# Kernel tuning notes

Hardware: AMD Instinct MI355X
Metric: run time of the kernel (lower is better)

Reference implementation:

```python
import jax, jax.numpy as jnp
import numpy as np

V = 50257   # vocab_size
D = 128     # embed_dim
B = 1024    # batch of center words
C = 10      # context window size


def setup_inputs() -> dict:
    key = jax.random.key(0)
    ks = jax.random.split(key, 12)
    s = 0.05  # small init scale for linear weights
    return {
        "center_id": jax.random.randint(ks[0], (B,), 0, V),
        "context_ids": jax.random.randint(ks[1], (B, C), 0, V),
        "epsilon": jax.random.normal(ks[2], (D,), dtype=jnp.float32),
        # embedding tables init uniform(-1, 1) as in the torch module
        "emb": jax.random.uniform(ks[3], (V, D), minval=-1.0, maxval=1.0, dtype=jnp.float32),
        "prior_means": jax.random.uniform(ks[4], (V, D), minval=-1.0, maxval=1.0, dtype=jnp.float32),
        "prior_vars": jax.random.uniform(ks[5], (V, D), minval=-1.0, maxval=1.0, dtype=jnp.float32),
        "W_enc": jax.random.normal(ks[6], (2 * D, 2 * D), dtype=jnp.float32) * s,
        "b_enc": jnp.zeros((2 * D,), dtype=jnp.float32),
        "W_mean": jax.random.normal(ks[7], (2 * D, D), dtype=jnp.float32) * s,
        "b_mean": jnp.zeros((D,), dtype=jnp.float32),
        "W_var": jax.random.normal(ks[8], (2 * D, D), dtype=jnp.float32) * s,
        "b_var": jnp.zeros((D,), dtype=jnp.float32),
        "W_vocab": jax.random.normal(ks[9], (D, V), dtype=jnp.float32) * s,
        "b_vocab": jnp.zeros((V,), dtype=jnp.float32),
    }


def reference(center_id, context_ids, epsilon, emb, prior_means, prior_vars,
              W_enc, b_enc, W_mean, b_mean, W_var, b_var, W_vocab, b_vocab):
    ce = emb[center_id]                       # [B, D]
    cx = emb[context_ids]                     # [B, C, D]
    enc_in = jnp.concatenate(
        [jnp.broadcast_to(ce[:, None, :], cx.shape), cx], axis=-1)  # [B, C, 2D]
    h = jax.nn.relu(enc_in @ W_enc + b_enc).sum(axis=1)  # [B, 2D]
    mean = h @ W_mean + b_mean                           # [B, D]
    var = jax.nn.softplus(h @ W_var + b_var)             # [B, D] (diag cov s0)
    z = mean + jnp.exp(var / 2.0) * epsilon              # single shared epsilon [D]
    logits = z @ W_vocab + b_vocab                        # [B, V]
    logp = jax.nn.log_softmax(logits, axis=1)             # log(categorical)

    pm = prior_means[center_id]                           # m1 [B, D]
    pv = jax.nn.softplus(prior_vars[center_id])           # diag cov s1 [B, D]
    diff = pm - mean
    # closed-form diagonal Gaussian KL, identical math to the
    # trace/inverse/det formulation over diagflat matrices in the source
    kl = 0.5 * jnp.sum(var / pv + diff * diff / pv - 1.0
                       + jnp.log(pv) - jnp.log(var), axis=1)  # [B]

    # reconstruction: sum_k log categorical[i, context_ids[i, k]]
    rec = jnp.take_along_axis(logp, context_ids, axis=1).sum(axis=1)  # [B]

    return jnp.mean(rec - kl)
```

## Files before the change

kernel.cpp:

```cpp
#include <hip/hip_runtime.h>
#include <math.h>

#define VV 50257
#define VPAD 50304
#define DD 128
#define BB 1024
#define CC 10

typedef short bf16x8 __attribute__((ext_vector_type(8)));
typedef float f32x4 __attribute__((ext_vector_type(4)));

__device__ inline float bf2f(unsigned short u) {
    return __uint_as_float(((unsigned)u) << 16);
}
__device__ inline unsigned short f2bf(float f) {
    unsigned u = __float_as_uint(f);
    unsigned r = ((u >> 16) & 1) + 0x7FFF;
    return (unsigned short)((u + r) >> 16);
}


__global__ __launch_bounds__(256) void k_prep0(
    const float* __restrict__ W_enc, const float* __restrict__ W_mean,
    const float* __restrict__ W_var, unsigned short* __restrict__ WeP,
    unsigned short* __restrict__ Wmv)
{
    __shared__ float tl[256][17];
    const int bid = blockIdx.x, tid = threadIdx.x;

    if (bid < 16) {
        const int jg = bid;
#pragma unroll
        for (int i = 0; i < 16; ++i) {
            int idx = i * 256 + tid;
            int k = idx >> 4, j = idx & 15;
            tl[k][j] = W_enc[(size_t)k * 256 + jg * 16 + j];
        }
        __syncthreads();
#pragma unroll
        for (int i = 0; i < 2; ++i) {
            int c = i * 256 + tid;
            int l15 = c & 15, q = (c >> 4) & 3, kI = c >> 6;
            bf16x8 o;
#pragma unroll
            for (int e = 0; e < 8; ++e)
                o[e] = (short)f2bf(tl[kI * 32 + q * 8 + e][l15]);
            *(bf16x8*)(WeP + (((size_t)jg * 8 + kI) * 64 + q * 16 + l15) * 8) = o;
        }
        return;
    }

    const int b4 = bid - 16;
#pragma unroll
    for (int i = 0; i < 32; ++i) {
        int idx = b4 * 8192 + i * 256 + tid;
        unsigned short m = f2bf(W_mean[idx]);
        unsigned short v = f2bf(W_var[idx]);
        *(ushort2*)(Wmv + (size_t)idx * 2) = make_ushort2(m, v);
    }
}

#define AS_STRIDE 520
__global__ __launch_bounds__(256) void k_main(
    const int* __restrict__ center_id, const int* __restrict__ context_ids,
    const float* __restrict__ emb, const unsigned short* __restrict__ WeP,
    const float* __restrict__ b_enc, const float* __restrict__ Wv,
    unsigned short* __restrict__ WvP, unsigned short* __restrict__ enc_relu)
{
    __shared__ __align__(16) unsigned char smraw[50688];
    const int bid = blockIdx.x, tid = threadIdx.x;

    if (bid >= 320) {
        float (*tile)[65] = (float (*)[65])smraw;
        const int s = bid - 320;
        const int v0 = s * 64;
#pragma unroll
        for (int i = 0; i < 32; ++i) {
            int idx = tid + i * 256;
            int k = idx >> 6, j = idx & 63;
            int v = v0 + j;
            tile[k][j] = (v < VV) ? Wv[(size_t)k * VV + v] : 0.f;
        }
        __syncthreads();
#pragma unroll
        for (int i = 0; i < 4; ++i) {
            int c = i * 256 + tid;
            int l15 = c & 15, q = (c >> 4) & 3, kI = (c >> 6) & 3, g = c >> 8;
            bf16x8 o;
#pragma unroll
            for (int e = 0; e < 8; ++e)
                o[e] = (short)f2bf(tile[kI * 32 + q * 8 + e][g * 16 + l15]);
            size_t vg = (size_t)s * 4 + g;
            *(bf16x8*)(WvP + ((vg * 4 + kI) * 64 + q * 16 + l15) * 8) = o;
        }
        return;
    }

    unsigned short* As = (unsigned short*)smraw;
    unsigned short (*Cs)[136] = (unsigned short (*)[136])(smraw + 33280);

    const int lane = tid & 63;
    const int wid  = tid >> 6;
    const int wm   = wid & 1;
    const int wn   = wid >> 1;
    const int quad = lane >> 4;
    const int l15  = lane & 15;

    const int bt = bid & 15;
    const int c  = (bid >> 4) % 10;
    const int zt = bid / 160;
    const int b0 = bt * 64;
    const int n0 = zt * 128;

    const int rlane = tid >> 4;
    const int c8    = tid & 15;
    const int kIc   = c8 >> 2, qc = c8 & 3;
#pragma unroll
    for (int p = 0; p < 4; ++p) {
        int r = p * 16 + rlane;
        int rid_ce = center_id[b0 + r];
        int rid_cx = context_ids[(b0 + r) * CC + c];
        const float* s0 = emb + (size_t)rid_ce * 128 + c8 * 8;
        const float* s1 = emb + (size_t)rid_cx * 128 + c8 * 8;
        float4 a0 = *(const float4*)s0, a1 = *(const float4*)(s0 + 4);
        float4 b0v = *(const float4*)s1, b1v = *(const float4*)(s1 + 4);
        bf16x8 oa, ob;
        oa[0] = (short)f2bf(a0.x); oa[1] = (short)f2bf(a0.y);
        oa[2] = (short)f2bf(a0.z); oa[3] = (short)f2bf(a0.w);
        oa[4] = (short)f2bf(a1.x); oa[5] = (short)f2bf(a1.y);
        oa[6] = (short)f2bf(a1.z); oa[7] = (short)f2bf(a1.w);
        ob[0] = (short)f2bf(b0v.x); ob[1] = (short)f2bf(b0v.y);
        ob[2] = (short)f2bf(b0v.z); ob[3] = (short)f2bf(b0v.w);
        ob[4] = (short)f2bf(b1v.x); ob[5] = (short)f2bf(b1v.y);
        ob[6] = (short)f2bf(b1v.z); ob[7] = (short)f2bf(b1v.w);
        *(bf16x8*)(As + (size_t)(p * 8 + kIc) * AS_STRIDE + (qc * 16 + rlane) * 8) = oa;
        *(bf16x8*)(As + (size_t)(p * 8 + kIc + 4) * AS_STRIDE + (qc * 16 + rlane) * 8) = ob;
    }
    __syncthreads();

    float benc[4];
#pragma unroll
    for (int nt = 0; nt < 4; ++nt)
        benc[nt] = b_enc[n0 + wn * 64 + nt * 16 + l15];

    f32x4 acc[2][4];
#pragma unroll
    for (int mt = 0; mt < 2; ++mt)
#pragma unroll
        for (int nt = 0; nt < 4; ++nt) acc[mt][nt] = (f32x4){0.f, 0.f, 0.f, 0.f};

#pragma unroll
    for (int kI = 0; kI < 8; ++kI) {
        bf16x8 a[2], b[4];
#pragma unroll
        for (int mt = 0; mt < 2; ++mt)
            a[mt] = *(const bf16x8*)(As + (size_t)((wm * 2 + mt) * 8 + kI) * AS_STRIDE + lane * 8);
#pragma unroll
        for (int nt = 0; nt < 4; ++nt) {
            size_t jg = (size_t)zt * 8 + wn * 4 + nt;
            b[nt] = *(const bf16x8*)(WeP + ((jg * 8 + kI) * 64 + lane) * 8);
        }
#pragma unroll
        for (int mt = 0; mt < 2; ++mt)
#pragma unroll
            for (int nt = 0; nt < 4; ++nt)
                acc[mt][nt] = __builtin_amdgcn_mfma_f32_16x16x32_bf16(
                    a[mt], b[nt], acc[mt][nt], 0, 0, 0);
    }

#pragma unroll
    for (int mt = 0; mt < 2; ++mt)
#pragma unroll
        for (int nt = 0; nt < 4; ++nt) {
            int col = wn * 64 + nt * 16 + l15;
#pragma unroll
            for (int reg = 0; reg < 4; ++reg) {
                int row = wm * 32 + mt * 16 + quad * 4 + reg;
                Cs[row][col] = f2bf(fmaxf(acc[mt][nt][reg] + benc[nt], 0.f));
            }
        }
    __syncthreads();
#pragma unroll
    for (int i = 0; i < 4; ++i) {
        int ch = i * 256 + tid;
        int row = ch >> 4, cc = ch & 15;
        bf16x8 v = *(const bf16x8*)&Cs[row][cc * 8];
        *(bf16x8*)(enc_relu + ((size_t)(b0 + row) * CC + c) * 256 + n0 + cc * 8) = v;
    }
}

__global__ __launch_bounds__(256) void k_latent(
    const unsigned short* __restrict__ enc_relu, const unsigned short* __restrict__ Wmv,
    const float* __restrict__ b_mean, const float* __restrict__ b_var,
    const float* __restrict__ epsilon,
    const int* __restrict__ center_id, const int* __restrict__ context_ids,
    const unsigned short* __restrict__ WvP, const float* __restrict__ bv,
    const float* __restrict__ prior_means, const float* __restrict__ prior_vars,
    unsigned short* __restrict__ z_pack, float* __restrict__ kl,
    float* __restrict__ ctxsum, float* __restrict__ out)
{
    __shared__ __align__(16) float hs[256];
    __shared__ float mpart[128], vpart[128];
    __shared__ float red[2];
    __shared__ float credp[CC][2];
    const int tid = threadIdx.x;
    const int b = blockIdx.x;

    if (b == 0 && tid == 0) out[0] = 0.f;

    {
        float s0 = 0.f;
#pragma unroll
        for (int c = 0; c < CC; ++c)
            s0 += bf2f(enc_relu[((size_t)b * CC + c) * 256 + tid]);
        hs[tid] = s0;
    }
    __syncthreads();

    const int d = tid & 127;
    const int half = tid >> 7;
    float m  = half ? 0.f : b_mean[d];
    float vr = half ? 0.f : b_var[d];
    const int kbase = half << 7;
    for (int k0 = 0; k0 < 128; k0 += 4) {
        float4 h4 = *(const float4*)&hs[kbase + k0];
#pragma unroll
        for (int kk = 0; kk < 4; ++kk) {
            float hk = ((const float*)&h4)[kk];
            ushort2 u = *(const ushort2*)(Wmv + ((size_t)(kbase + k0 + kk) * 128 + d) * 2);
            m  += hk * bf2f(u.x);
            vr += hk * bf2f(u.y);
        }
    }
    if (half) { mpart[d] = m; vpart[d] = vr; }
    __syncthreads();

    if (!half) {
        const int wid = tid >> 6;
        m  += mpart[d];
        vr += vpart[d];

        float var = (vr > 20.f) ? vr : log1pf(__expf(vr));
        float zd = m + __expf(0.5f * var) * epsilon[d];
        unsigned short zu = f2bf(zd);
        const int kIz = d >> 5, qz = (d >> 3) & 3, ez = d & 7;
        {
            const int bg = b >> 4, l15b = b & 15;
            z_pack[(((size_t)(bg * 4 + kIz)) * 64 + qz * 16 + l15b) * 8 + ez] = zu;
        }
        float zb = bf2f(zu);

        int cid = center_id[b];
        float pm  = prior_means[(size_t)cid * 128 + d];
        float pvr = prior_vars[(size_t)cid * 128 + d];
        float pv  = (pvr > 20.f) ? pvr : log1pf(__expf(pvr));
        float diff = pm - m;
        float t = var / pv + diff * diff / pv - 1.f + logf(pv) - logf(var);
#pragma unroll
        for (int off = 32; off; off >>= 1) t += __shfl_down(t, off, 64);
        if ((tid & 63) == 0) red[wid] = t;

        int cids[CC];
#pragma unroll
        for (int p = 0; p < CC; ++p) cids[p] = context_ids[b * CC + p];
        float cs[CC];
#pragma unroll
        for (int p = 0; p < CC; ++p) {
            int vg = cids[p] >> 4, l15v = cids[p] & 15;
            float w = bf2f(WvP[(((size_t)(vg * 4 + kIz)) * 64 + qz * 16 + l15v) * 8 + ez]);
            cs[p] = zb * w;
        }
#pragma unroll
        for (int p = 0; p < CC; ++p) {
#pragma unroll
            for (int off = 32; off; off >>= 1) cs[p] += __shfl_down(cs[p], off, 64);
        }
        if ((tid & 63) == 0) {
#pragma unroll
            for (int p = 0; p < CC; ++p) credp[p][wid] = cs[p];
        }
    }
    __syncthreads();
    if (tid == 0) {
        kl[b] = 0.5f * (red[0] + red[1]);
        float c = 0.f;
        int cid0;
#pragma unroll
        for (int p = 0; p < CC; ++p) {
            cid0 = context_ids[b * CC + p];
            c += credp[p][0] + credp[p][1] + bv[cid0];
        }
        ctxsum[b] = c;
    }
}

__global__ __launch_bounds__(256) void k_lse(
    const unsigned short* __restrict__ z_pack, const unsigned short* __restrict__ WvP,
    const float* __restrict__ bv, float* __restrict__ partial)
{
    __shared__ float pl[2][128][20];
    const int x = blockIdx.x + 8 * blockIdx.y;
    if (x >= 393) return;
    const int mg = blockIdx.z;

    const int tid  = threadIdx.x;
    const int lane = tid & 63;
    const int wid  = tid >> 6;
    const int wm   = wid & 1;
    const int wn   = wid >> 1;
    const int quad = lane >> 4;
    const int l15  = lane & 15;
    const int n0   = x * 128;

    bf16x8 bfr[4][4];
#pragma unroll
    for (int nt = 0; nt < 4; ++nt) {
        size_t vg = (size_t)x * 8 + wn * 4 + nt;
#pragma unroll
        for (int kI = 0; kI < 4; ++kI)
            bfr[nt][kI] = *(const bf16x8*)(WvP + ((vg * 4 + kI) * 64 + lane) * 8);
    }

    float bvf[4];
#pragma unroll
    for (int nt = 0; nt < 4; ++nt) {
        int n = n0 + wn * 64 + nt * 16 + l15;
        bvf[nt] = (n < VV) ? bv[n] : -__builtin_huge_valf();
    }

#pragma unroll
    for (int mi = 0; mi < 2; ++mi) {
        const int mi_g = mg * 2 + mi;

        f32x4 acc[4][4];
#pragma unroll
        for (int mt = 0; mt < 4; ++mt)
#pragma unroll
            for (int nt = 0; nt < 4; ++nt) acc[mt][nt] = (f32x4){0.f, 0.f, 0.f, 0.f};

#pragma unroll
        for (int kI = 0; kI < 4; ++kI) {
            bf16x8 afr[4];
#pragma unroll
            for (int mt = 0; mt < 4; ++mt) {
                size_t bg = (size_t)mi_g * 8 + wm * 4 + mt;
                afr[mt] = *(const bf16x8*)(z_pack + ((bg * 4 + kI) * 64 + lane) * 8);
            }
#pragma unroll
            for (int mt = 0; mt < 4; ++mt)
#pragma unroll
                for (int nt = 0; nt < 4; ++nt)
                    acc[mt][nt] = __builtin_amdgcn_mfma_f32_16x16x32_bf16(
                        afr[mt], bfr[nt][kI], acc[mt][nt], 0, 0, 0);
        }

#pragma unroll
        for (int mt = 0; mt < 4; ++mt)
#pragma unroll
            for (int reg = 0; reg < 4; ++reg) {
                float s = 0.f;
#pragma unroll
                for (int nt = 0; nt < 4; ++nt)
                    s += __expf(acc[mt][nt][reg] + bvf[nt]);
                pl[wn][wm * 64 + mt * 16 + quad * 4 + reg][l15] = s;
            }
        __syncthreads();
        if (tid < 128) {
            const float* p0 = &pl[0][tid][0];
            const float* p1 = &pl[1][tid][0];
            float4 a0 = *(const float4*)(p0);
            float4 a1 = *(const float4*)(p0 + 4);
            float4 a2 = *(const float4*)(p0 + 8);
            float4 a3 = *(const float4*)(p0 + 12);
            float4 b0 = *(const float4*)(p1);
            float4 b1 = *(const float4*)(p1 + 4);
            float4 b2 = *(const float4*)(p1 + 8);
            float4 b3 = *(const float4*)(p1 + 12);
            float tot = (a0.x + a0.y + a0.z + a0.w) + (a1.x + a1.y + a1.z + a1.w)
                      + (a2.x + a2.y + a2.z + a2.w) + (a3.x + a3.y + a3.z + a3.w)
                      + (b0.x + b0.y + b0.z + b0.w) + (b1.x + b1.y + b1.z + b1.w)
                      + (b2.x + b2.y + b2.z + b2.w) + (b3.x + b3.y + b3.z + b3.w);
            partial[(size_t)x * 1024 + mi_g * 128 + tid] = tot;
        }
        __syncthreads();
    }
}

__global__ __launch_bounds__(256) void k_reduce(
    const float* __restrict__ partial, const float* __restrict__ ctxsum,
    const float* __restrict__ kl, float* __restrict__ out)
{
    __shared__ float bred[4];
    const int tid = threadIdx.x;
    const int row = blockIdx.x * 16 + (tid >> 4);
    const int part = tid & 15;

    float s = 0.f;
    for (int vb = part; vb < 393; vb += 16)
        s += partial[(size_t)vb * 1024 + row];
    s += __shfl_xor(s, 1, 64);
    s += __shfl_xor(s, 2, 64);
    s += __shfl_xor(s, 4, 64);
    s += __shfl_xor(s, 8, 64);

    float v = 0.f;
    if (part == 0)
        v = ctxsum[row] - 10.f * logf(s) - kl[row];
    v += __shfl_xor(v, 16, 64);
    v += __shfl_xor(v, 32, 64);
    if ((tid & 63) == 0) bred[tid >> 6] = v;
    __syncthreads();
    if (tid == 0)
        atomicAdd(out, (bred[0] + bred[1] + bred[2] + bred[3]) * (1.f / 1024.f));
}

extern "C" void kernel_launch(void* const* d_in, const int* in_sizes, int n_in,
                              void* d_out, int out_size, void* d_ws, size_t ws_size,
                              hipStream_t stream)
{
    const int*   center_id   = (const int*)d_in[0];
    const int*   context_ids = (const int*)d_in[1];
    const float* epsilon     = (const float*)d_in[2];
    const float* emb         = (const float*)d_in[3];
    const float* prior_means = (const float*)d_in[4];
    const float* prior_vars  = (const float*)d_in[5];
    const float* W_enc       = (const float*)d_in[6];
    const float* b_enc       = (const float*)d_in[7];
    const float* W_mean      = (const float*)d_in[8];
    const float* b_mean      = (const float*)d_in[9];
    const float* W_var       = (const float*)d_in[10];
    const float* b_var       = (const float*)d_in[11];
    const float* W_vocab     = (const float*)d_in[12];
    const float* b_vocab     = (const float*)d_in[13];

    float* out = (float*)d_out;
    char*  ws  = (char*)d_ws;

    size_t off = 0;
    unsigned short* WvP      = (unsigned short*)(ws + off); off += 12877824;
    unsigned short* WeP      = (unsigned short*)(ws + off); off += 131072;
    unsigned short* Wmv      = (unsigned short*)(ws + off); off += 131072;
    unsigned short* z_pack   = (unsigned short*)(ws + off); off += 262144;
    unsigned short* enc_relu = (unsigned short*)(ws + off); off += 5242880;
    float*          kl       = (float*)(ws + off);          off += 4096;
    float*          ctxsum   = (float*)(ws + off);          off += 4096;
    float*          partial  = (float*)(ws + off);          off += 1609728;

    k_prep0<<<20, 256, 0, stream>>>(W_enc, W_mean, W_var, WeP, Wmv);
    k_main<<<1106, 256, 0, stream>>>(center_id, context_ids, emb, WeP, b_enc,
                                     W_vocab, WvP, enc_relu);
    k_latent<<<1024, 256, 0, stream>>>(enc_relu, Wmv, b_mean, b_var, epsilon,
                                       center_id, context_ids, WvP, b_vocab,
                                       prior_means, prior_vars, z_pack, kl,
                                       ctxsum, out);
    k_lse<<<dim3(8, 50, 4), 256, 0, stream>>>(z_pack, WvP, b_vocab, partial);
    k_reduce<<<64, 256, 0, stream>>>(partial, ctxsum, kl, out);
}
```

Measured before the change: 200.2 us.

## Batch four rows per latent block and move W_mean/W_var packing into main kernel

The latent kernel now handles four batch rows per 512-thread block. Each Wmv weight load is reused across four rows, the K dimension is split four ways, and the context-logit gather is spread across all eight waves. The W_mean/W_var bf16 packing moves out of the prep kernel into four extra blocks of the main kernel, leaving the prep kernel with only the W_enc transpose. The aim is to cut redundant weight reads and per-block overhead in the latent stage. The cost is more shared memory and extra syncs per block, and fewer blocks (256) to fill the GPU.

New measurement: 201.1 us. No clear change (+0.4%).

```diff
diff --git a/kernel.cpp b/kernel.cpp
--- a/kernel.cpp
+++ b/kernel.cpp
@@ -21,42 +21,26 @@
 
 
 __global__ __launch_bounds__(256) void k_prep0(
-    const float* __restrict__ W_enc, const float* __restrict__ W_mean,
-    const float* __restrict__ W_var, unsigned short* __restrict__ WeP,
-    unsigned short* __restrict__ Wmv)
+    const float* __restrict__ W_enc, unsigned short* __restrict__ WeP)
 {
     __shared__ float tl[256][17];
-    const int bid = blockIdx.x, tid = threadIdx.x;
-
-    if (bid < 16) {
-        const int jg = bid;
-#pragma unroll
-        for (int i = 0; i < 16; ++i) {
-            int idx = i * 256 + tid;
-            int k = idx >> 4, j = idx & 15;
-            tl[k][j] = W_enc[(size_t)k * 256 + jg * 16 + j];
-        }
-        __syncthreads();
-#pragma unroll
-        for (int i = 0; i < 2; ++i) {
-            int c = i * 256 + tid;
-            int l15 = c & 15, q = (c >> 4) & 3, kI = c >> 6;
-            bf16x8 o;
-#pragma unroll
-            for (int e = 0; e < 8; ++e)
-                o[e] = (short)f2bf(tl[kI * 32 + q * 8 + e][l15]);
-            *(bf16x8*)(WeP + (((size_t)jg * 8 + kI) * 64 + q * 16 + l15) * 8) = o;
-        }
-        return;
-    }
-
-    const int b4 = bid - 16;
-#pragma unroll
-    for (int i = 0; i < 32; ++i) {
-        int idx = b4 * 8192 + i * 256 + tid;
-        unsigned short m = f2bf(W_mean[idx]);
-        unsigned short v = f2bf(W_var[idx]);
-        *(ushort2*)(Wmv + (size_t)idx * 2) = make_ushort2(m, v);
+    const int jg = blockIdx.x, tid = threadIdx.x;
+#pragma unroll
+    for (int i = 0; i < 16; ++i) {
+        int idx = i * 256 + tid;
+        int k = idx >> 4, j = idx & 15;
+        tl[k][j] = W_enc[(size_t)k * 256 + jg * 16 + j];
+    }
+    __syncthreads();
+#pragma unroll
+    for (int i = 0; i < 2; ++i) {
+        int c = i * 256 + tid;
+        int l15 = c & 15, q = (c >> 4) & 3, kI = c >> 6;
+        bf16x8 o;
+#pragma unroll
+        for (int e = 0; e < 8; ++e)
+            o[e] = (short)f2bf(tl[kI * 32 + q * 8 + e][l15]);
+        *(bf16x8*)(WeP + (((size_t)jg * 8 + kI) * 64 + q * 16 + l15) * 8) = o;
     }
 }
 
@@ -65,10 +49,24 @@
     const int* __restrict__ center_id, const int* __restrict__ context_ids,
     const float* __restrict__ emb, const unsigned short* __restrict__ WeP,
     const float* __restrict__ b_enc, const float* __restrict__ Wv,
-    unsigned short* __restrict__ WvP, unsigned short* __restrict__ enc_relu)
+    const float* __restrict__ W_mean, const float* __restrict__ W_var,
+    unsigned short* __restrict__ WvP, unsigned short* __restrict__ Wmv,
+    unsigned short* __restrict__ enc_relu)
 {
     __shared__ __align__(16) unsigned char smraw[50688];
     const int bid = blockIdx.x, tid = threadIdx.x;
+
+    if (bid >= 1106) {
+        const int b4 = bid - 1106;
+#pragma unroll
+        for (int i = 0; i < 32; ++i) {
+            int idx = b4 * 8192 + i * 256 + tid;
+            unsigned short m = f2bf(W_mean[idx]);
+            unsigned short v = f2bf(W_var[idx]);
+            *(ushort2*)(Wmv + (size_t)idx * 2) = make_ushort2(m, v);
+        }
+        return;
+    }
 
     if (bid >= 320) {
         float (*tile)[65] = (float (*)[65])smraw;
@@ -189,7 +187,7 @@
     }
 }
 
-__global__ __launch_bounds__(256) void k_latent(
+__global__ __launch_bounds__(512) void k_latent(
     const unsigned short* __restrict__ enc_relu, const unsigned short* __restrict__ Wmv,
     const float* __restrict__ b_mean, const float* __restrict__ b_var,
     const float* __restrict__ epsilon,
@@ -199,98 +197,125 @@
     unsigned short* __restrict__ z_pack, float* __restrict__ kl,
     float* __restrict__ ctxsum, float* __restrict__ out)
 {
-    __shared__ __align__(16) float hs[256];
-    __shared__ float mpart[128], vpart[128];
-    __shared__ float red[2];
-    __shared__ float credp[CC][2];
+    __shared__ __align__(16) float hs[4][256];
+    __shared__ float mpart[3][4][128], vpart[3][4][128];
+    __shared__ float zsh[4][128];
+    __shared__ float red[4][2];
+    __shared__ float credw[4][2];
     const int tid = threadIdx.x;
-    const int b = blockIdx.x;
-
-    if (b == 0 && tid == 0) out[0] = 0.f;
+    const int b0 = blockIdx.x * 4;
+
+    if (blockIdx.x == 0 && tid == 0) out[0] = 0.f;
 
     {
-        float s0 = 0.f;
-#pragma unroll
-        for (int c = 0; c < CC; ++c)
-            s0 += bf2f(enc_relu[((size_t)b * CC + c) * 256 + tid]);
-        hs[tid] = s0;
-    }
-    __syncthreads();
-
-    const int d = tid & 127;
-    const int half = tid >> 7;
-    float m  = half ? 0.f : b_mean[d];
-    float vr = half ? 0.f : b_var[d];
-    const int kbase = half << 7;
-    for (int k0 = 0; k0 < 128; k0 += 4) {
-        float4 h4 = *(const float4*)&hs[kbase + k0];
+        const int col = tid & 255;
+        const int rr  = tid >> 8;
+#pragma unroll
+        for (int r2 = 0; r2 < 2; ++r2) {
+            int row = rr * 2 + r2;
+            float s = 0.f;
+#pragma unroll
+            for (int c = 0; c < CC; ++c)
+                s += bf2f(enc_relu[((size_t)(b0 + row) * CC + c) * 256 + col]);
+            hs[row][col] = s;
+        }
+    }
+    __syncthreads();
+
+    const int d    = tid & 127;
+    const int part = tid >> 7;
+    const int kbase = part * 64;
+    float m[4], vr[4];
+#pragma unroll
+    for (int r = 0; r < 4; ++r) {
+        m[r]  = part ? 0.f : b_mean[d];
+        vr[r] = part ? 0.f : b_var[d];
+    }
+    for (int k0 = 0; k0 < 64; k0 += 4) {
+        float4 h4[4];
+#pragma unroll
+        for (int r = 0; r < 4; ++r)
+            h4[r] = *(const float4*)&hs[r][kbase + k0];
 #pragma unroll
         for (int kk = 0; kk < 4; ++kk) {
-            float hk = ((const float*)&h4)[kk];
             ushort2 u = *(const ushort2*)(Wmv + ((size_t)(kbase + k0 + kk) * 128 + d) * 2);
-            m  += hk * bf2f(u.x);
-            vr += hk * bf2f(u.y);
-        }
-    }
-    if (half) { mpart[d] = m; vpart[d] = vr; }
-    __syncthreads();
-
-    if (!half) {
+            float wm_ = bf2f(u.x), wv_ = bf2f(u.y);
+#pragma unroll
+            for (int r = 0; r < 4; ++r) {
+                float hk = ((const float*)&h4[r])[kk];
+                m[r]  += hk * wm_;
+                vr[r] += hk * wv_;
+            }
+        }
+    }
+    if (part) {
+#pragma unroll
+        for (int r = 0; r < 4; ++r) {
+            mpart[part - 1][r][d] = m[r];
+            vpart[part - 1][r][d] = vr[r];
+        }
+    }
+    __syncthreads();
+
+    if (tid < 128) {
         const int wid = tid >> 6;
-        m  += mpart[d];
-        vr += vpart[d];
-
-        float var = (vr > 20.f) ? vr : log1pf(__expf(vr));
-        float zd = m + __expf(0.5f * var) * epsilon[d];
-        unsigned short zu = f2bf(zd);
         const int kIz = d >> 5, qz = (d >> 3) & 3, ez = d & 7;
-        {
-            const int bg = b >> 4, l15b = b & 15;
+        const int bg = b0 >> 4;
+#pragma unroll
+        for (int r = 0; r < 4; ++r) {
+            float mm = m[r]  + mpart[0][r][d] + mpart[1][r][d] + mpart[2][r][d];
+            float vv = vr[r] + vpart[0][r][d] + vpart[1][r][d] + vpart[2][r][d];
+
+            float var = (vv > 20.f) ? vv : log1pf(__expf(vv));
+            float zd = mm + __expf(0.5f * var) * epsilon[d];
+            unsigned short zu = f2bf(zd);
+            const int bb = b0 + r;
+            const int l15b = bb & 15;
             z_pack[(((size_t)(bg * 4 + kIz)) * 64 + qz * 16 + l15b) * 8 + ez] = zu;
-        }
-        float zb = bf2f(zu);
-
-        int cid = center_id[b];
-        float pm  = prior_means[(size_t)cid * 128 + d];
-        float pvr = prior_vars[(size_t)cid * 128 + d];
-        float pv  = (pvr > 20.f) ? pvr : log1pf(__expf(pvr));
-        float diff = pm - m;
-        float t = var / pv + diff * diff / pv - 1.f + logf(pv) - logf(var);
-#pragma unroll
-        for (int off = 32; off; off >>= 1) t += __shfl_down(t, off, 64);
-        if ((tid & 63) == 0) red[wid] = t;
-
-        int cids[CC];
-#pragma unroll
-        for (int p = 0; p < CC; ++p) cids[p] = context_ids[b * CC + p];
-        float cs[CC];
-#pragma unroll
-        for (int p = 0; p < CC; ++p) {
-            int vg = cids[p] >> 4, l15v = cids[p] & 15;
-            float w = bf2f(WvP[(((size_t)(vg * 4 + kIz)) * 64 + qz * 16 + l15v) * 8 + ez]);
-            cs[p] = zb * w;
-        }
-#pragma unroll
-        for (int p = 0; p < CC; ++p) {
-#pragma unroll
-            for (int off = 32; off; off >>= 1) cs[p] += __shfl_down(cs[p], off, 64);
-        }
-        if ((tid & 63) == 0) {
-#pragma unroll
-            for (int p = 0; p < CC; ++p) credp[p][wid] = cs[p];
-        }
-    }
-    __syncthreads();
-    if (tid == 0) {
-        kl[b] = 0.5f * (red[0] + red[1]);
-        float c = 0.f;
-        int cid0;
-#pragma unroll
-        for (int p = 0; p < CC; ++p) {
-            cid0 = context_ids[b * CC + p];
-            c += credp[p][0] + credp[p][1] + bv[cid0];
-        }
-        ctxsum[b] = c;
+            zsh[r][d] = bf2f(zu);
+
+            int cid = center_id[bb];
+            float pm  = prior_means[(size_t)cid * 128 + d];
+            float pvr = prior_vars[(size_t)cid * 128 + d];
+            float pv  = (pvr > 20.f) ? pvr : log1pf(__expf(pvr));
+            float diff = pm - mm;
+            float t = var / pv + diff * diff / pv - 1.f + logf(pv) - logf(var);
+#pragma unroll
+            for (int off = 32; off; off >>= 1) t += __shfl_xor(t, off, 64);
+            if ((tid & 63) == 0) red[r][wid] = t;
+        }
+    }
+    __syncthreads();
+
+    {
+        const int w     = tid >> 6;
+        const int row   = w & 3;
+        const int phalf = w >> 2;
+        const int lane  = tid & 63;
+        const float z1 = zsh[row][lane];
+        const float z2 = zsh[row][lane + 64];
+        const int kI1 = lane >> 5, q1 = (lane >> 3) & 3, e1 = lane & 7;
+        const int d2  = lane + 64;
+        const int kI2 = d2 >> 5,  q2 = (d2 >> 3) & 3,  e2 = d2 & 7;
+        float cacc = 0.f;
+#pragma unroll
+        for (int pp = 0; pp < 5; ++pp) {
+            int p = phalf * 5 + pp;
+            int cid = context_ids[(b0 + row) * CC + p];
+            int vg = cid >> 4, l15v = cid & 15;
+            float w1 = bf2f(WvP[(((size_t)(vg * 4 + kI1)) * 64 + q1 * 16 + l15v) * 8 + e1]);
+            float w2 = bf2f(WvP[(((size_t)(vg * 4 + kI2)) * 64 + q2 * 16 + l15v) * 8 + e2]);
+            float cs = z1 * w1 + z2 * w2;
+#pragma unroll
+            for (int off = 32; off; off >>= 1) cs += __shfl_xor(cs, off, 64);
+            cacc += cs + bv[cid];
+        }
+        if (lane == 0) credw[row][phalf] = cacc;
+    }
+    __syncthreads();
+    if (tid < 4) {
+        kl[b0 + tid]     = 0.5f * (red[tid][0] + red[tid][1]);
+        ctxsum[b0 + tid] = credw[tid][0] + credw[tid][1];
     }
 }
 
@@ -446,13 +471,13 @@
     float*          ctxsum   = (float*)(ws + off);          off += 4096;
     float*          partial  = (float*)(ws + off);          off += 1609728;
 
-    k_prep0<<<20, 256, 0, stream>>>(W_enc, W_mean, W_var, WeP, Wmv);
-    k_main<<<1106, 256, 0, stream>>>(center_id, context_ids, emb, WeP, b_enc,
-                                     W_vocab, WvP, enc_relu);
-    k_latent<<<1024, 256, 0, stream>>>(enc_relu, Wmv, b_mean, b_var, epsilon,
-                                       center_id, context_ids, WvP, b_vocab,
-                                       prior_means, prior_vars, z_pack, kl,
-                                       ctxsum, out);
+    k_prep0<<<16, 256, 0, stream>>>(W_enc, WeP);
+    k_main<<<1110, 256, 0, stream>>>(center_id, context_ids, emb, WeP, b_enc,
+                                     W_vocab, W_mean, W_var, WvP, Wmv, enc_relu);
+    k_latent<<<256, 512, 0, stream>>>(enc_relu, Wmv, b_mean, b_var, epsilon,
+                                      center_id, context_ids, WvP, b_vocab,
+                                      prior_means, prior_vars, z_pack, kl,
+                                      ctxsum, out);
     k_lse<<<dim3(8, 50, 4), 256, 0, stream>>>(z_pack, WvP, b_vocab, partial);
     k_reduce<<<64, 256, 0, stream>>>(partial, ctxsum, kl, out);
 }
```
